# Optimization experiments

Measured on AMD Instinct MI355X. Metric: run time of the kernel, lower is better.

## Reference

```python
import jax, jax.numpy as jnp
import numpy as np

B, DIM, H, W = 32, 256, 64, 64
WIN, SHIFT, HEADS = 8, 4, 8
HEAD_DIM = DIM // HEADS
SCALE = HEAD_DIM ** -0.5
N = WIN * WIN


def _window_partition(x, ws):
    # x: (B, H, W, C) -> (B*nW, ws, ws, C)
    b, h, w, c = x.shape
    x = x.reshape(b, h // ws, ws, w // ws, ws, c)
    return x.transpose(0, 1, 3, 2, 4, 5).reshape(-1, ws, ws, c)


def _window_reverse(windows, ws, h, w):
    # windows: (B*nW, ws, ws, C) -> (B, H, W, C)
    b = windows.shape[0] // ((h // ws) * (w // ws))
    x = windows.reshape(b, h // ws, w // ws, ws, ws, -1)
    return x.transpose(0, 1, 3, 2, 4, 5).reshape(b, h, w, -1)


def _rel_pos_index(ws):
    coords = np.stack(np.meshgrid(np.arange(ws), np.arange(ws), indexing='ij'))  # (2,ws,ws)
    cf = coords.reshape(2, -1)
    rel = cf[:, :, None] - cf[:, None, :]  # (2,N,N)
    rel = rel.transpose(1, 2, 0)
    rel[:, :, 0] += ws - 1
    rel[:, :, 1] += ws - 1
    rel[:, :, 0] *= 2 * ws - 1
    return rel.sum(-1)  # (N,N) int


def _shift_mask(h, w, ws, shift):
    img_mask = np.zeros((1, h, w, 1), np.float32)
    slices = (slice(0, -ws), slice(-ws, -shift), slice(-shift, None))
    cnt = 0
    for hs in slices:
        for wsl in slices:
            img_mask[:, hs, wsl, :] = cnt
            cnt += 1
    mw = np.asarray(_window_partition(jnp.asarray(img_mask), ws)).reshape(-1, ws * ws)
    am = mw[:, None, :] - mw[:, :, None]  # (nW, N, N)
    return jnp.asarray(np.where(am != 0, -100.0, 0.0).astype(np.float32))


_REL_IDX = jnp.asarray(_rel_pos_index(WIN).reshape(-1))  # (N*N,)
_ATTN_MASK = _shift_mask(H, W, WIN, SHIFT)  # (nW, N, N)


def setup_inputs() -> dict:
    key = jax.random.key(0)
    k1, k2, k3, k4 = jax.random.split(key, 4)
    x = jax.random.normal(k1, (B, DIM, H, W), jnp.float32)
    qkv_w = jax.random.normal(k2, (DIM, 3 * DIM), jnp.float32) * (DIM ** -0.5)
    qkv_b = jax.random.normal(k3, (3 * DIM,), jnp.float32) * 0.02
    rel_bias_table = jax.random.normal(k4, ((2 * WIN - 1) ** 2, HEADS), jnp.float32) * 0.02
    return {"x": x, "qkv_w": qkv_w, "qkv_b": qkv_b, "rel_bias_table": rel_bias_table}


def reference(x, qkv_w, qkv_b, rel_bias_table):
    b, c, h, w = x.shape
    xp = x.transpose(0, 2, 3, 1)  # (B,H,W,C)
    xs = jnp.roll(xp, (-SHIFT, -SHIFT), axis=(1, 2))
    win = _window_partition(xs, WIN).reshape(-1, N, c)  # (BW,N,C)
    bw = win.shape[0]
    qkv = win @ qkv_w + qkv_b  # (BW,N,3C)
    qkv = qkv.reshape(bw, N, 3, HEADS, HEAD_DIM).transpose(2, 0, 3, 1, 4)
    q, k, v = qkv[0], qkv[1], qkv[2]  # (BW,heads,N,hd)
    attn = jnp.einsum('whnd,whmd->whnm', q * SCALE, k)  # (BW,heads,N,N)
    bias = rel_bias_table[_REL_IDX].reshape(N, N, HEADS).transpose(2, 0, 1)  # (heads,N,N)
    attn = attn + bias[None]
    n_win = _ATTN_MASK.shape[0]
    attn = attn.reshape(b, n_win, HEADS, N, N) + _ATTN_MASK[None, :, None]
    attn = jax.nn.softmax(attn.reshape(bw, HEADS, N, N), axis=-1)
    out = jnp.einsum('whnm,whmd->whnd', attn, v)  # (BW,heads,N,hd)
    out = out.transpose(0, 2, 1, 3).reshape(bw, N, DIM)
    out = out.reshape(-1, WIN, WIN, DIM)
    out = _window_reverse(out, WIN, h, w)  # (B,H,W,C)
    out = jnp.roll(out, (SHIFT, SHIFT), axis=(1, 2))
    return out.transpose(0, 3, 1, 2)  # (B,C,H,W)
```

## Files before the change

kernel.cpp:

```cpp
#include <hip/hip_runtime.h>


typedef __attribute__((ext_vector_type(8))) short short8;
typedef __attribute__((ext_vector_type(4))) float f32x4;

static __device__ __forceinline__ short f2bf(float f) {
    unsigned u = __float_as_uint(f);
    u = (u + 0x7fffu + ((u >> 16) & 1u)) >> 16;
    return (short)u;
}

static __device__ __forceinline__ int region(int i) {
    return (i < 56) ? 0 : ((i < 60) ? 1 : 2);
}

__global__ void wt_transpose(const float* __restrict__ w, unsigned short* __restrict__ wt) {
    int col = blockIdx.x;
    int k   = threadIdx.x;
    float v = w[k * 768 + col];
    unsigned u = __float_as_uint(v);
    u = (u + 0x7fffu + ((u >> 16) & 1u)) >> 16;
    wt[col * 256 + k] = (unsigned short)u;
}

__global__ __launch_bounds__(256, 4) void swin_kernel(
    const float* __restrict__ x,
    const unsigned short* __restrict__ wt,
    const float* __restrict__ qkv_b,
    const float* __restrict__ tbl,
    float* __restrict__ out)
{
    __shared__ char smem[40192];
    unsigned short* w_s  = (unsigned short*)(smem);
    unsigned short* q_s  = (unsigned short*)(smem + 25344);
    unsigned short* k_s  = (unsigned short*)(smem + 30464);
    unsigned short* vt_s = (unsigned short*)(smem + 35584);
    unsigned short* p_s  = (unsigned short*)(smem);
    float*          o_s  = (float*)(smem + 9216);

    const int tid  = threadIdx.x;
    const int wave = tid >> 6;
    const int lane = tid & 63;
    const int ln   = lane & 15;
    const int quad = lane >> 4;

    const int g    = blockIdx.x;
    const int xcd  = g & 7;
    const int j    = g >> 3;
    const int ww   = j & 7;
    const int band = xcd * 32 + (j >> 3);
    const int b    = band >> 3;
    const int wh   = band & 7;

    const int t_a  = wave * 16 + ln;
    const int ti_a = t_a >> 3, tj_a = t_a & 7;
    const int si = (wh * 8 + ti_a + 4) & 63;
    const int sj = (ww * 8 + tj_a + 4) & 63;
    const float* xb = x + ((size_t)b * 256) * 4096 + si * 64 + sj;
    short8 afrag[8];
    #pragma unroll
    for (int ks = 0; ks < 8; ++ks) {
        #pragma unroll
        for (int jj = 0; jj < 8; ++jj) {
            int c = ks * 32 + quad * 8 + jj;
            afrag[ks][jj] = f2bf(xb[(size_t)c * 4096]);
        }
    }

    const int row0 = wave * 16 + quad * 4;

    for (int h = 0; h < 8; ++h) {
        #pragma unroll
        for (int half = 0; half < 2; ++half) {
            __syncthreads();

            #pragma unroll
            for (int i = 0; i < 6; ++i) {
                int idx = i * 256 + tid;
                int cl  = idx >> 5;
                int ch  = idx & 31;
                int colL = half * 48 + cl;
                int col  = ((colL >> 5) << 8) + (h << 5) + (colL & 31);
                short8 wv = *(const short8*)(wt + col * 256 + ch * 8);
                *(short8*)(w_s + cl * 264 + ch * 8) = wv;
            }
            __syncthreads();

            f32x4 acc[3];
            #pragma unroll
            for (int jt = 0; jt < 3; ++jt) acc[jt] = (f32x4){0.f, 0.f, 0.f, 0.f};
            #pragma unroll
            for (int ks = 0; ks < 8; ++ks) {
                short8 a = afrag[ks];
                #pragma unroll
                for (int jt = 0; jt < 3; ++jt) {
                    short8 bb = *(const short8*)(w_s + (jt * 16 + ln) * 264 + ks * 32 + quad * 8);
                    acc[jt] = __builtin_amdgcn_mfma_f32_16x16x32_bf16(a, bb, acc[jt], 0, 0, 0);
                }
            }
            #pragma unroll
            for (int jt = 0; jt < 3; ++jt) {
                int colL = half * 48 + jt * 16 + ln;
                int seg  = (half * 48 + jt * 16) >> 5;
                int cc   = colL & 31;
                float bias = qkv_b[(seg << 8) + (h << 5) + cc];
                #pragma unroll
                for (int r = 0; r < 4; ++r) {
                    float v = acc[jt][r] + bias;
                    int tok = row0 + r;
                    if (seg == 0)      q_s[tok * 40 + cc] = (unsigned short)f2bf(v * 0.17677669529663689f);
                    else if (seg == 1) k_s[tok * 40 + cc] = (unsigned short)f2bf(v);
                    else               vt_s[cc * 72 + tok] = (unsigned short)f2bf(v);
                }
            }
        }
        __syncthreads();

        short8 aq = *(const short8*)(q_s + (wave * 16 + ln) * 40 + quad * 8);
        f32x4 sacc[4];
        #pragma unroll
        for (int nt = 0; nt < 4; ++nt) {
            short8 bk = *(const short8*)(k_s + (nt * 16 + ln) * 40 + quad * 8);
            f32x4 z = (f32x4){0.f, 0.f, 0.f, 0.f};
            sacc[nt] = __builtin_amdgcn_mfma_f32_16x16x32_bf16(aq, bk, z, 0, 0, 0);
        }
        float sv[4][4];
        #pragma unroll
        for (int nt = 0; nt < 4; ++nt) {
            int tk = nt * 16 + ln;
            int tik = tk >> 3, tjk = tk & 7;
            int cntk = region(wh * 8 + tik) * 3 + region(ww * 8 + tjk);
            #pragma unroll
            for (int r = 0; r < 4; ++r) {
                int tq = row0 + r;
                int tiq = tq >> 3, tjq = tq & 7;
                int idx = (tiq - tik + 7) * 15 + (tjq - tjk + 7);
                int cntq = region(wh * 8 + tiq) * 3 + region(ww * 8 + tjq);
                float s = sacc[nt][r] + tbl[idx * 8 + h];
                if (cntq != cntk) s -= 100.0f;
                sv[nt][r] = s;
            }
        }
        #pragma unroll
        for (int r = 0; r < 4; ++r) {
            float m = fmaxf(fmaxf(sv[0][r], sv[1][r]), fmaxf(sv[2][r], sv[3][r]));
            m = fmaxf(m, __shfl_xor(m, 1, 64));
            m = fmaxf(m, __shfl_xor(m, 2, 64));
            m = fmaxf(m, __shfl_xor(m, 4, 64));
            m = fmaxf(m, __shfl_xor(m, 8, 64));
            float p0 = __expf(sv[0][r] - m);
            float p1 = __expf(sv[1][r] - m);
            float p2 = __expf(sv[2][r] - m);
            float p3 = __expf(sv[3][r] - m);
            float ssum = p0 + p1 + p2 + p3;
            ssum += __shfl_xor(ssum, 1, 64);
            ssum += __shfl_xor(ssum, 2, 64);
            ssum += __shfl_xor(ssum, 4, 64);
            ssum += __shfl_xor(ssum, 8, 64);
            float inv = 1.0f / ssum;
            int pr = (row0 + r) * 72;
            p_s[pr +      ln] = (unsigned short)f2bf(p0 * inv);
            p_s[pr + 16 + ln] = (unsigned short)f2bf(p1 * inv);
            p_s[pr + 32 + ln] = (unsigned short)f2bf(p2 * inv);
            p_s[pr + 48 + ln] = (unsigned short)f2bf(p3 * inv);
        }

        f32x4 oacc[2];
        oacc[0] = (f32x4){0.f, 0.f, 0.f, 0.f};
        oacc[1] = (f32x4){0.f, 0.f, 0.f, 0.f};
        #pragma unroll
        for (int ks = 0; ks < 2; ++ks) {
            short8 ap = *(const short8*)(p_s + (wave * 16 + ln) * 72 + ks * 32 + quad * 8);
            #pragma unroll
            for (int nt = 0; nt < 2; ++nt) {
                short8 bv = *(const short8*)(vt_s + (nt * 16 + ln) * 72 + ks * 32 + quad * 8);
                oacc[nt] = __builtin_amdgcn_mfma_f32_16x16x32_bf16(ap, bv, oacc[nt], 0, 0, 0);
            }
        }
        #pragma unroll
        for (int nt = 0; nt < 2; ++nt)
            #pragma unroll
            for (int r = 0; r < 4; ++r)
                o_s[(row0 + r) * 33 + nt * 16 + ln] = oacc[nt][r];
        __syncthreads();

        {
            int cl  = tid & 31;
            int ti2 = tid >> 5;
            f32x4 v0, v1;
            #pragma unroll
            for (int tj = 0; tj < 4; ++tj) v0[tj] = o_s[(ti2 * 8 + tj) * 33 + cl];
            #pragma unroll
            for (int tj = 0; tj < 4; ++tj) v1[tj] = o_s[(ti2 * 8 + 4 + tj) * 33 + cl];
            int c  = (h << 5) + cl;
            int di = (wh * 8 + ti2 + 4) & 63;
            float* op = out + ((size_t)(b * 256 + c)) * 4096 + di * 64;
            *(f32x4*)(op + (ww * 8 + 4))        = v0;
            *(f32x4*)(op + ((ww * 8 + 8) & 63)) = v1;
        }
    }
}

extern "C" void kernel_launch(void* const* d_in, const int* in_sizes, int n_in,
                              void* d_out, int out_size, void* d_ws, size_t ws_size,
                              hipStream_t stream) {
    const float* x      = (const float*)d_in[0];
    const float* qkv_w  = (const float*)d_in[1];
    const float* qkv_b  = (const float*)d_in[2];
    const float* tbl    = (const float*)d_in[3];
    float* out          = (float*)d_out;
    unsigned short* Wt  = (unsigned short*)d_ws;

    wt_transpose<<<dim3(768), dim3(256), 0, stream>>>(qkv_w, Wt);
    swin_kernel<<<dim3(2048), dim3(256), 0, stream>>>(x, Wt, qkv_b, tbl, out);
}
```

Measured before the change: 457.5 us.

## Process two windows per block to reuse staged QKV weights, DPP reductions

Each block now handles two adjacent windows, with each wave owning 32 tokens (two MFMA row tiles). Every weight tile staged into shared memory therefore feeds twice as many MFMAs, and the grid is halved. The output goes straight from registers to global as float4 stores, which drops the o_s staging buffer and a barrier per head. V^T is stored with an XOR swizzle, and the softmax row reductions use DPP row rotates instead of shuffles. In exchange the kernel uses more shared memory and registers, with launch bounds lowered to 3 blocks per CU.

```diff
diff --git a/kernel.cpp b/kernel.cpp
--- a/kernel.cpp
+++ b/kernel.cpp
@@ -1,8 +1,9 @@
 #include <hip/hip_runtime.h>
 
 
-typedef __attribute__((ext_vector_type(8))) short short8;
-typedef __attribute__((ext_vector_type(4))) float f32x4;
+typedef short short8  __attribute__((ext_vector_type(8)));
+typedef short short4v __attribute__((ext_vector_type(4)));
+typedef float f32x4   __attribute__((ext_vector_type(4)));
 
 static __device__ __forceinline__ short f2bf(float f) {
     unsigned u = __float_as_uint(f);
@@ -12,6 +13,23 @@
 
 static __device__ __forceinline__ int region(int i) {
     return (i < 56) ? 0 : ((i < 60) ? 1 : 2);
+}
+
+#define DPP_ROR(x, n) __int_as_float(__builtin_amdgcn_update_dpp( \
+    0, __float_as_int(x), 0x120 + (n), 0xF, 0xF, true))
+static __device__ __forceinline__ float row16_max(float v) {
+    v = fmaxf(v, DPP_ROR(v, 1));
+    v = fmaxf(v, DPP_ROR(v, 2));
+    v = fmaxf(v, DPP_ROR(v, 4));
+    v = fmaxf(v, DPP_ROR(v, 8));
+    return v;
+}
+static __device__ __forceinline__ float row16_sum(float v) {
+    v += DPP_ROR(v, 1);
+    v += DPP_ROR(v, 2);
+    v += DPP_ROR(v, 4);
+    v += DPP_ROR(v, 8);
+    return v;
 }
 
 __global__ void wt_transpose(const float* __restrict__ w, unsigned short* __restrict__ wt) {
@@ -23,20 +41,19 @@
     wt[col * 256 + k] = (unsigned short)u;
 }
 
-__global__ __launch_bounds__(256, 4) void swin_kernel(
+__global__ __launch_bounds__(256, 3) void swin_kernel(
     const float* __restrict__ x,
     const unsigned short* __restrict__ wt,
     const float* __restrict__ qkv_b,
     const float* __restrict__ tbl,
     float* __restrict__ out)
 {
-    __shared__ char smem[40192];
+    __shared__ char smem[54016];
     unsigned short* w_s  = (unsigned short*)(smem);
     unsigned short* q_s  = (unsigned short*)(smem + 25344);
-    unsigned short* k_s  = (unsigned short*)(smem + 30464);
-    unsigned short* vt_s = (unsigned short*)(smem + 35584);
+    unsigned short* k_s  = (unsigned short*)(smem + 35584);
+    unsigned short* vt_s = (unsigned short*)(smem + 45824);
     unsigned short* p_s  = (unsigned short*)(smem);
-    float*          o_s  = (float*)(smem + 9216);
 
     const int tid  = threadIdx.x;
     const int wave = tid >> 6;
@@ -46,28 +63,36 @@
 
     const int g    = blockIdx.x;
     const int xcd  = g & 7;
-    const int j    = g >> 3;
-    const int ww   = j & 7;
-    const int band = xcd * 32 + (j >> 3);
+    const int jj   = g >> 3;
+    const int wb   = jj & 3;
+    const int band = xcd * 32 + (jj >> 2);
     const int b    = band >> 3;
     const int wh   = band & 7;
-
-    const int t_a  = wave * 16 + ln;
-    const int ti_a = t_a >> 3, tj_a = t_a & 7;
-    const int si = (wh * 8 + ti_a + 4) & 63;
-    const int sj = (ww * 8 + tj_a + 4) & 63;
-    const float* xb = x + ((size_t)b * 256) * 4096 + si * 64 + sj;
-    short8 afrag[8];
+    const int ww0  = wb * 2;
+
+    const int win = wave >> 1;
+    const int rb  = (wave & 1) * 32;
+    const int wwA = ww0 + win;
+
+    unsigned short* qw = q_s  + win * 2560;
+    unsigned short* kw = k_s  + win * 2560;
+    unsigned short* vw = vt_s + win * 2048;
+    unsigned short* pw = p_s  + win * 4608;
+
+    short8 afrag[2][8];
     #pragma unroll
-    for (int ks = 0; ks < 8; ++ks) {
-        #pragma unroll
-        for (int jj = 0; jj < 8; ++jj) {
-            int c = ks * 32 + quad * 8 + jj;
-            afrag[ks][jj] = f2bf(xb[(size_t)c * 4096]);
-        }
+    for (int mt = 0; mt < 2; ++mt) {
+        int t  = rb + mt * 16 + ln;
+        int ti = t >> 3, tj = t & 7;
+        int si = (wh * 8 + ti + 4) & 63;
+        int sj = (wwA * 8 + tj + 4) & 63;
+        const float* xb = x + ((size_t)b * 256) * 4096 + si * 64 + sj;
+        #pragma unroll
+        for (int ks = 0; ks < 8; ++ks)
+            #pragma unroll
+            for (int j = 0; j < 8; ++j)
+                afrag[mt][ks][j] = f2bf(xb[(size_t)(ks * 32 + quad * 8 + j) * 4096]);
     }
-
-    const int row0 = wave * 16 + quad * 4;
 
     for (int h = 0; h < 8; ++h) {
         #pragma unroll
@@ -81,122 +106,131 @@
                 int ch  = idx & 31;
                 int colL = half * 48 + cl;
                 int col  = ((colL >> 5) << 8) + (h << 5) + (colL & 31);
-                short8 wv = *(const short8*)(wt + col * 256 + ch * 8);
-                *(short8*)(w_s + cl * 264 + ch * 8) = wv;
+                *(short8*)(w_s + cl * 264 + ch * 8) =
+                    *(const short8*)(wt + col * 256 + ch * 8);
             }
             __syncthreads();
 
-            f32x4 acc[3];
-            #pragma unroll
-            for (int jt = 0; jt < 3; ++jt) acc[jt] = (f32x4){0.f, 0.f, 0.f, 0.f};
+            f32x4 acc[2][3];
+            #pragma unroll
+            for (int mt = 0; mt < 2; ++mt)
+                #pragma unroll
+                for (int jt = 0; jt < 3; ++jt) acc[mt][jt] = (f32x4){0.f,0.f,0.f,0.f};
             #pragma unroll
             for (int ks = 0; ks < 8; ++ks) {
-                short8 a = afrag[ks];
                 #pragma unroll
                 for (int jt = 0; jt < 3; ++jt) {
                     short8 bb = *(const short8*)(w_s + (jt * 16 + ln) * 264 + ks * 32 + quad * 8);
-                    acc[jt] = __builtin_amdgcn_mfma_f32_16x16x32_bf16(a, bb, acc[jt], 0, 0, 0);
+                    acc[0][jt] = __builtin_amdgcn_mfma_f32_16x16x32_bf16(afrag[0][ks], bb, acc[0][jt], 0, 0, 0);
+                    acc[1][jt] = __builtin_amdgcn_mfma_f32_16x16x32_bf16(afrag[1][ks], bb, acc[1][jt], 0, 0, 0);
                 }
             }
             #pragma unroll
             for (int jt = 0; jt < 3; ++jt) {
-                int colL = half * 48 + jt * 16 + ln;
-                int seg  = (half * 48 + jt * 16) >> 5;
-                int cc   = colL & 31;
+                const int seg = (half == 0) ? (jt < 2 ? 0 : 1) : (jt == 0 ? 1 : 2);
+                int cc = ((half * 48 + jt * 16) & 31) + ln;
                 float bias = qkv_b[(seg << 8) + (h << 5) + cc];
                 #pragma unroll
-                for (int r = 0; r < 4; ++r) {
-                    float v = acc[jt][r] + bias;
-                    int tok = row0 + r;
-                    if (seg == 0)      q_s[tok * 40 + cc] = (unsigned short)f2bf(v * 0.17677669529663689f);
-                    else if (seg == 1) k_s[tok * 40 + cc] = (unsigned short)f2bf(v);
-                    else               vt_s[cc * 72 + tok] = (unsigned short)f2bf(v);
+                for (int mt = 0; mt < 2; ++mt) {
+                    int t0 = rb + mt * 16 + quad * 4;
+                    if (seg == 0) {
+                        #pragma unroll
+                        for (int r = 0; r < 4; ++r)
+                            qw[(t0 + r) * 40 + cc] =
+                                (unsigned short)f2bf((acc[mt][jt][r] + bias) * 0.17677669529663689f);
+                    } else if (seg == 1) {
+                        #pragma unroll
+                        for (int r = 0; r < 4; ++r)
+                            kw[(t0 + r) * 40 + cc] = (unsigned short)f2bf(acc[mt][jt][r] + bias);
+                    } else {
+                        short4v pk;
+                        #pragma unroll
+                        for (int r = 0; r < 4; ++r) pk[r] = f2bf(acc[mt][jt][r] + bias);
+                        int u = ((t0 >> 3) ^ (cc & 7)) << 3;
+                        *(short4v*)(vw + cc * 64 + u + (t0 & 7)) = pk;
+                    }
                 }
             }
         }
         __syncthreads();
 
-        short8 aq = *(const short8*)(q_s + (wave * 16 + ln) * 40 + quad * 8);
-        f32x4 sacc[4];
-        #pragma unroll
-        for (int nt = 0; nt < 4; ++nt) {
-            short8 bk = *(const short8*)(k_s + (nt * 16 + ln) * 40 + quad * 8);
-            f32x4 z = (f32x4){0.f, 0.f, 0.f, 0.f};
-            sacc[nt] = __builtin_amdgcn_mfma_f32_16x16x32_bf16(aq, bk, z, 0, 0, 0);
-        }
-        float sv[4][4];
-        #pragma unroll
-        for (int nt = 0; nt < 4; ++nt) {
-            int tk = nt * 16 + ln;
-            int tik = tk >> 3, tjk = tk & 7;
-            int cntk = region(wh * 8 + tik) * 3 + region(ww * 8 + tjk);
+        short8 bk[4];
+        #pragma unroll
+        for (int nt = 0; nt < 4; ++nt)
+            bk[nt] = *(const short8*)(kw + (nt * 16 + ln) * 40 + quad * 8);
+
+        #pragma unroll
+        for (int mt = 0; mt < 2; ++mt) {
+            int t0 = rb + mt * 16;
+            short8 aq = *(const short8*)(qw + (t0 + ln) * 40 + quad * 8);
+            f32x4 sacc[4];
+            #pragma unroll
+            for (int nt = 0; nt < 4; ++nt) {
+                f32x4 z = (f32x4){0.f, 0.f, 0.f, 0.f};
+                sacc[nt] = __builtin_amdgcn_mfma_f32_16x16x32_bf16(aq, bk[nt], z, 0, 0, 0);
+            }
+            float sv[4][4];
+            #pragma unroll
+            for (int nt = 0; nt < 4; ++nt) {
+                int tk  = nt * 16 + ln;
+                int tik = tk >> 3, tjk = tk & 7;
+                int cntk = region(wh * 8 + tik) * 3 + region(wwA * 8 + tjk);
+                #pragma unroll
+                for (int r = 0; r < 4; ++r) {
+                    int tq  = t0 + quad * 4 + r;
+                    int tiq = tq >> 3, tjq = tq & 7;
+                    int idx = (tiq - tik + 7) * 15 + (tjq - tjk + 7);
+                    int cntq = region(wh * 8 + tiq) * 3 + region(wwA * 8 + tjq);
+                    float s = sacc[nt][r] + tbl[idx * 8 + h];
+                    if (cntq != cntk) s -= 100.0f;
+                    sv[nt][r] = s;
+                }
+            }
             #pragma unroll
             for (int r = 0; r < 4; ++r) {
-                int tq = row0 + r;
-                int tiq = tq >> 3, tjq = tq & 7;
-                int idx = (tiq - tik + 7) * 15 + (tjq - tjk + 7);
-                int cntq = region(wh * 8 + tiq) * 3 + region(ww * 8 + tjq);
-                float s = sacc[nt][r] + tbl[idx * 8 + h];
-                if (cntq != cntk) s -= 100.0f;
-                sv[nt][r] = s;
-            }
-        }
-        #pragma unroll
-        for (int r = 0; r < 4; ++r) {
-            float m = fmaxf(fmaxf(sv[0][r], sv[1][r]), fmaxf(sv[2][r], sv[3][r]));
-            m = fmaxf(m, __shfl_xor(m, 1, 64));
-            m = fmaxf(m, __shfl_xor(m, 2, 64));
-            m = fmaxf(m, __shfl_xor(m, 4, 64));
-            m = fmaxf(m, __shfl_xor(m, 8, 64));
-            float p0 = __expf(sv[0][r] - m);
-            float p1 = __expf(sv[1][r] - m);
-            float p2 = __expf(sv[2][r] - m);
-            float p3 = __expf(sv[3][r] - m);
-            float ssum = p0 + p1 + p2 + p3;
-            ssum += __shfl_xor(ssum, 1, 64);
-            ssum += __shfl_xor(ssum, 2, 64);
-            ssum += __shfl_xor(ssum, 4, 64);
-            ssum += __shfl_xor(ssum, 8, 64);
-            float inv = 1.0f / ssum;
-            int pr = (row0 + r) * 72;
-            p_s[pr +      ln] = (unsigned short)f2bf(p0 * inv);
-            p_s[pr + 16 + ln] = (unsigned short)f2bf(p1 * inv);
-            p_s[pr + 32 + ln] = (unsigned short)f2bf(p2 * inv);
-            p_s[pr + 48 + ln] = (unsigned short)f2bf(p3 * inv);
-        }
-
-        f32x4 oacc[2];
-        oacc[0] = (f32x4){0.f, 0.f, 0.f, 0.f};
-        oacc[1] = (f32x4){0.f, 0.f, 0.f, 0.f};
-        #pragma unroll
-        for (int ks = 0; ks < 2; ++ks) {
-            short8 ap = *(const short8*)(p_s + (wave * 16 + ln) * 72 + ks * 32 + quad * 8);
-            #pragma unroll
-            for (int nt = 0; nt < 2; ++nt) {
-                short8 bv = *(const short8*)(vt_s + (nt * 16 + ln) * 72 + ks * 32 + quad * 8);
-                oacc[nt] = __builtin_amdgcn_mfma_f32_16x16x32_bf16(ap, bv, oacc[nt], 0, 0, 0);
-            }
-        }
-        #pragma unroll
-        for (int nt = 0; nt < 2; ++nt)
-            #pragma unroll
-            for (int r = 0; r < 4; ++r)
-                o_s[(row0 + r) * 33 + nt * 16 + ln] = oacc[nt][r];
-        __syncthreads();
-
-        {
-            int cl  = tid & 31;
-            int ti2 = tid >> 5;
-            f32x4 v0, v1;
-            #pragma unroll
-            for (int tj = 0; tj < 4; ++tj) v0[tj] = o_s[(ti2 * 8 + tj) * 33 + cl];
-            #pragma unroll
-            for (int tj = 0; tj < 4; ++tj) v1[tj] = o_s[(ti2 * 8 + 4 + tj) * 33 + cl];
-            int c  = (h << 5) + cl;
-            int di = (wh * 8 + ti2 + 4) & 63;
-            float* op = out + ((size_t)(b * 256 + c)) * 4096 + di * 64;
-            *(f32x4*)(op + (ww * 8 + 4))        = v0;
-            *(f32x4*)(op + ((ww * 8 + 8) & 63)) = v1;
+                float m = fmaxf(fmaxf(sv[0][r], sv[1][r]), fmaxf(sv[2][r], sv[3][r]));
+                m = row16_max(m);
+                float p0 = __expf(sv[0][r] - m);
+                float p1 = __expf(sv[1][r] - m);
+                float p2 = __expf(sv[2][r] - m);
+                float p3 = __expf(sv[3][r] - m);
+                float ssum = row16_sum(p0 + p1 + p2 + p3);
+                float inv = 1.0f / ssum;
+                int pr = (t0 + quad * 4 + r) * 72;
+                pw[pr +      ln] = (unsigned short)f2bf(p0 * inv);
+                pw[pr + 16 + ln] = (unsigned short)f2bf(p1 * inv);
+                pw[pr + 32 + ln] = (unsigned short)f2bf(p2 * inv);
+                pw[pr + 48 + ln] = (unsigned short)f2bf(p3 * inv);
+            }
+
+            f32x4 oacc[2];
+            oacc[0] = (f32x4){0.f, 0.f, 0.f, 0.f};
+            oacc[1] = (f32x4){0.f, 0.f, 0.f, 0.f};
+            #pragma unroll
+            for (int ks2 = 0; ks2 < 2; ++ks2) {
+                short8 ap = *(const short8*)(pw + (t0 + ln) * 72 + ks2 * 32 + quad * 8);
+                #pragma unroll
+                for (int nt2 = 0; nt2 < 2; ++nt2) {
+                    int cc = nt2 * 16 + ln;
+                    int u  = ((ks2 * 4 + quad) ^ (cc & 7)) << 3;
+                    short8 bv = *(const short8*)(vw + cc * 64 + u);
+                    oacc[nt2] = __builtin_amdgcn_mfma_f32_16x16x32_bf16(ap, bv, oacc[nt2], 0, 0, 0);
+                }
+            }
+            {
+                int t0r = t0 + quad * 4;
+                int ti  = t0r >> 3, tj0 = t0r & 7;
+                int di  = (wh * 8 + ti + 4) & 63;
+                int dj0 = (wwA * 8 + tj0 + 4) & 63;
+                #pragma unroll
+                for (int nt2 = 0; nt2 < 2; ++nt2) {
+                    int c = (h << 5) + nt2 * 16 + ln;
+                    f32x4 ov;
+                    #pragma unroll
+                    for (int r = 0; r < 4; ++r) ov[r] = oacc[nt2][r];
+                    *(f32x4*)(out + ((size_t)(b * 256 + c)) * 4096 + di * 64 + dj0) = ov;
+                }
+            }
         }
     }
 }
@@ -212,5 +246,5 @@
     unsigned short* Wt  = (unsigned short*)d_ws;
 
     wt_transpose<<<dim3(768), dim3(256), 0, stream>>>(qkv_w, Wt);
-    swin_kernel<<<dim3(2048), dim3(256), 0, stream>>>(x, Wt, qkv_b, tbl, out);
-}
+    swin_kernel<<<dim3(1024), dim3(256), 0, stream>>>(x, Wt, qkv_b, tbl, out);
+}
```

Result: slower. 549.1 us (+20.0%).
